# Performance work log

Measured on AMD Instinct MI355X. Metric: run time of the kernel, lower is better.

## Reference

```python
import jax, jax.numpy as jnp
import numpy as np

B, D, L, E, RH, EH = 8192, 1024, 3, 8, 128, 256  # batch, dim, levels, experts, router hidden, expert hidden


def setup_inputs() -> dict:
    key = jax.random.key(0)
    ks = jax.random.split(key, 9)
    s_d = 1.0 / np.sqrt(D)
    s_rh = 1.0 / np.sqrt(RH)
    s_eh = 1.0 / np.sqrt(EH)
    return {
        "x": jax.random.normal(ks[0], (B, D), dtype=jnp.float32),
        # routers: Linear(D,128) -> ReLU -> Linear(128,E) -> softmax, one per level
        "router_w1": jax.random.uniform(ks[1], (L, D, RH), jnp.float32, -s_d, s_d),
        "router_b1": jax.random.uniform(ks[2], (L, RH), jnp.float32, -s_d, s_d),
        "router_w2": jax.random.uniform(ks[3], (L, RH, E), jnp.float32, -s_rh, s_rh),
        "router_b2": jax.random.uniform(ks[4], (L, E), jnp.float32, -s_rh, s_rh),
        # experts: Linear(D,256) -> ReLU -> Linear(256,D), E per level
        "expert_w1": jax.random.uniform(ks[5], (L, E, D, EH), jnp.float32, -s_d, s_d),
        "expert_b1": jax.random.uniform(ks[6], (L, E, EH), jnp.float32, -s_d, s_d),
        "expert_w2": jax.random.uniform(ks[7], (L, E, EH, D), jnp.float32, -s_eh, s_eh),
        "expert_b2": jax.random.uniform(ks[8], (L, E, D), jnp.float32, -s_eh, s_eh),
    }


def _forward(x, router_w1, router_b1, router_w2, router_b2,
             expert_w1, expert_b1, expert_w2, expert_b2):
    def level(cur, params):
        rw1, rb1, rw2, rb2, ew1, eb1, ew2, eb2 = params
        # router: [B,E] softmax weights
        rh = jax.nn.relu(cur @ rw1 + rb1)
        w = jax.nn.softmax(rh @ rw2 + rb2, axis=-1)
        # dense all-expert eval: grouped GEMMs
        h = jax.nn.relu(jnp.einsum("bd,edh->beh", cur, ew1) + eb1)  # [B,E,EH]
        y = jnp.einsum("beh,ehd->bed", h, ew2) + eb2                # [B,E,D]
        out = jnp.einsum("be,bed->bd", w, y)                        # softmax-weighted sum
        return out, None

    out, _ = jax.lax.scan(
        level, x,
        (router_w1, router_b1, router_w2, router_b2,
         expert_w1, expert_b1, expert_w2, expert_b2))
    return out


def reference(x, router_w1, router_b1, router_w2, router_b2,
              expert_w1, expert_b1, expert_w2, expert_b2):
    return _forward(x, router_w1, router_b1, router_w2, router_b2,
                    expert_w1, expert_b1, expert_w2, expert_b2)
```

## Files before the change

kernel.cpp:

```cpp
#include <hip/hip_runtime.h>
#include <stdint.h>

#define BB   8192
#define DD   1024
#define EE   8
#define RHH  128
#define EHH  256
#define NE1  2048
#define KX   2112

using f32x4  = __attribute__((ext_vector_type(4))) float;
using bf16x8 = __attribute__((ext_vector_type(8))) __bf16;

__device__ __forceinline__ unsigned short f2bf(float f) {
    union { float f; uint32_t u; } v; v.f = f;
    uint32_t u = v.u;
    uint32_t r = (u + 0x7FFFu + ((u >> 16) & 1u)) >> 16;
    return (unsigned short)r;
}
__device__ __forceinline__ float bf2f(unsigned short h) {
    union { uint32_t u; float f; } v; v.u = ((uint32_t)h) << 16;
    return v.f;
}

__device__ __forceinline__ void llds16(void* l, const void* g) {
    __builtin_amdgcn_global_load_lds(
        (const __attribute__((address_space(1))) uint32_t*)g,
        (__attribute__((address_space(3))) uint32_t*)l, 16, 0, 0);
}

__device__ __forceinline__ void rawbar() {
    asm volatile("" ::: "memory");
    __builtin_amdgcn_s_barrier();
    asm volatile("" ::: "memory");
}

template<int N> __device__ __forceinline__ void vmwait() {
    asm volatile("s_waitcnt vmcnt(%0)" :: "n"(N) : "memory");
}

#define MFMA16(a,b,c) __builtin_amdgcn_mfma_f32_16x16x32_bf16(a,b,c,0,0,0)

__device__ __forceinline__ void prep512(float (*T)[65], int pbid, int tid,
    const float* __restrict__ rw1, const float* __restrict__ ew1,
    const float* __restrict__ ew2, const float* __restrict__ eb2,
    unsigned short* __restrict__ rw1t, unsigned short* __restrict__ W1t,
    unsigned short* __restrict__ W2t)
{
    const int hl = tid & 63, gq = tid >> 6;
    if (pbid < 512) {
        int e = pbid >> 6, kt = (pbid >> 2) & 15, ht = pbid & 3;
        const float* src = ew1 + ((size_t)e << 18);
#pragma unroll
        for (int i = 0; i < 8; ++i) {
            int kl = i * 8 + gq;
            T[kl][hl] = src[(size_t)(kt * 64 + kl) * 256 + ht * 64 + hl];
        }
        __syncthreads();
#pragma unroll
        for (int i = 0; i < 8; ++i) {
            int hl2 = i * 8 + gq;
            int n = e * 256 + ht * 64 + hl2;
            W1t[(size_t)n * 1024 + kt * 64 + hl] = f2bf(T[hl][hl2]);
        }
    } else if (pbid < 1024) {
        int b2 = pbid - 512;
        int npt = b2 >> 4, dt = b2 & 15;
#pragma unroll
        for (int i = 0; i < 8; ++i) {
            int npl = i * 8 + gq;
            T[npl][hl] = ew2[(size_t)(npt * 64 + npl) * 1024 + dt * 64 + hl];
        }
        __syncthreads();
#pragma unroll
        for (int i = 0; i < 8; ++i) {
            int dl2 = i * 8 + gq;
            int d = dt * 64 + dl2;
            W2t[(size_t)d * KX + npt * 64 + hl] = f2bf(T[hl][dl2]);
        }
    } else if (pbid < 1056) {
        int b2 = pbid - 1024;
        int dt = b2 >> 1, ht = b2 & 1;
#pragma unroll
        for (int i = 0; i < 8; ++i) {
            int dl = i * 8 + gq;
            T[dl][hl] = rw1[(size_t)(dt * 64 + dl) * 128 + ht * 64 + hl];
        }
        __syncthreads();
#pragma unroll
        for (int i = 0; i < 8; ++i) {
            int hl2 = i * 8 + gq;
            int h = ht * 64 + hl2;
            rw1t[(size_t)h * 1024 + dt * 64 + hl] = f2bf(T[hl][hl2]);
        }
    } else if (pbid < 1058) {
        int d = (pbid - 1056) * 512 + tid;
        unsigned short vv[8];
#pragma unroll
        for (int e = 0; e < 8; ++e) vv[e] = f2bf(eb2[(size_t)e * 1024 + d]);
        *(uint4*)&W2t[(size_t)d * KX + NE1] = *(const uint4*)vv;
    } else {
        int d = (pbid - 1058) * 512 + tid;
        uint4 z = make_uint4(0, 0, 0, 0);
#pragma unroll
        for (int j = 0; j < 7; ++j)
            *(uint4*)&W2t[(size_t)d * KX + NE1 + 8 + j * 8] = z;
    }
}

__global__ __launch_bounds__(512) void mega0(
    const float* __restrict__ x, unsigned short* __restrict__ xb,
    unsigned short* __restrict__ Hb,
    const float* __restrict__ rw1, const float* __restrict__ ew1,
    const float* __restrict__ ew2, const float* __restrict__ eb2,
    unsigned short* __restrict__ rw1t, unsigned short* __restrict__ W1t,
    unsigned short* __restrict__ W2t)
{
    __shared__ float T[64][65];
    const int bid = blockIdx.x, tid = threadIdx.x;
    if (bid < 2048) {
        size_t idx = (size_t)bid * 512 + tid;
        const float* p = x + idx * 8;
        uint32_t w[4];
#pragma unroll
        for (int j = 0; j < 4; ++j)
            w[j] = (uint32_t)f2bf(p[2 * j]) | ((uint32_t)f2bf(p[2 * j + 1]) << 16);
        *(uint4*)(xb + idx * 8) = make_uint4(w[0], w[1], w[2], w[3]);
    } else if (bid < 2064) {
        int row = (bid - 2048) * 512 + tid;
        uint4 z = make_uint4(0, 0, 0, 0);
        unsigned short* p = Hb + (size_t)row * KX + NE1 + EE;
#pragma unroll
        for (int j = 0; j < 7; ++j)
            *(uint4*)(p + j * 8) = z;
    } else {
        prep512(T, bid - 2064, tid, rw1, ew1, ew2, eb2, rw1t, W1t, W2t);
    }
}

__global__ __launch_bounds__(512) void prep_lvl512(
    const float* __restrict__ rw1, const float* __restrict__ ew1,
    const float* __restrict__ ew2, const float* __restrict__ eb2,
    unsigned short* __restrict__ rw1t, unsigned short* __restrict__ W1t,
    unsigned short* __restrict__ W2t)
{
    __shared__ float T[64][65];
    prep512(T, blockIdx.x, threadIdx.x, rw1, ew1, ew2, eb2, rw1t, W1t, W2t);
}

__global__ __launch_bounds__(512, 2) void router_prep(
    const unsigned short* __restrict__ xb, const unsigned short* __restrict__ rw1t,
    const float* __restrict__ rw2, const float* __restrict__ rb1,
    const float* __restrict__ rb2, float* __restrict__ wbuf,
    unsigned short* __restrict__ Hb,
    const float* __restrict__ rw1_n, const float* __restrict__ ew1_n,
    const float* __restrict__ ew2_n, const float* __restrict__ eb2_n,
    unsigned short* __restrict__ rw1t_n, unsigned short* __restrict__ W1t_n,
    unsigned short* __restrict__ W2t_n)
{
    __shared__ __align__(16) char SR[73728];
    const int bid = blockIdx.x;
    const int tid = threadIdx.x;

    if (bid >= 128) {
        prep512((float (*)[65])SR, bid - 128, tid, rw1_n, ew1_n, ew2_n, eb2_n,
                rw1t_n, W1t_n, W2t_n);
        return;
    }

    const int lane = tid & 63, wv = tid >> 6;
    const int g = wv >> 2, wq = wv & 3;
    const int l16 = lane & 15, lhi = lane >> 4;
    const long m0 = (long)bid * 64;

    const int r0 = tid >> 2, sl = tid & 3;
    const int sg = sl ^ ((r0 >> 1) & 3);

    const int xrow = (tid >> 2) & 63, xkg = tid >> 8;
    const char* xsrc = (const char*)xb + (m0 + xrow) * 2048 + xkg * 1024 + sg * 16;
    const char* wsrc = (const char*)rw1t + (long)r0 * 2048 + sg * 16;

    f32x4 acc[8];
    const f32x4 zero = {0.f, 0.f, 0.f, 0.f};
#pragma unroll
    for (int i = 0; i < 8; ++i) acc[i] = zero;

    auto stage = [&](int buf, int t) {
        char* base = SR + buf * 24576;
        llds16(base + tid * 16, xsrc + t * 64);
        llds16(base + 8192 + tid * 16, wsrc + t * 64);
        llds16(base + 16384 + tid * 16, wsrc + 1024 + t * 64);
    };

    stage(0, 0); stage(1, 1);

    const int swz = (l16 >> 1) & 3;
    const int aoff = g * 2048 + (wq * 16 + l16) * 32 + ((lhi ^ swz) << 3);
    const int boff = 4096 + g * 4096 + l16 * 32 + ((lhi ^ swz) << 3);

    int cb = 0, sb = 2;
    for (int t = 0; t < 16; ++t) {
        if (t < 15) vmwait<3>(); else vmwait<0>();
        rawbar();
        const unsigned short* bufp = (const unsigned short*)(SR + cb * 24576);
        bf16x8 aF = *(const bf16x8*)&bufp[aoff];
        bf16x8 bF[8];
#pragma unroll
        for (int ni = 0; ni < 8; ++ni)
            bF[ni] = *(const bf16x8*)&bufp[boff + ni * 512];
        if (t + 2 < 16) stage(sb, t + 2);
        __builtin_amdgcn_s_setprio(1);
#pragma unroll
        for (int ni = 0; ni < 8; ++ni)
            acc[ni] = MFMA16(aF, bF[ni], acc[ni]);
        __builtin_amdgcn_s_setprio(0);
        cb = (cb + 1 == 3) ? 0 : cb + 1;
        sb = (sb + 1 == 3) ? 0 : sb + 1;
    }

    rawbar();

    float* rhs = (float*)SR;
    float* lg  = (float*)(SR + 64 * 132 * 4);

    if (g == 1) {
#pragma unroll
        for (int ni = 0; ni < 8; ++ni)
#pragma unroll
            for (int rr = 0; rr < 4; ++rr)
                rhs[(wq * 16 + lhi * 4 + rr) * 132 + ni * 16 + l16] = acc[ni][rr];
    }
    rawbar();
    if (g == 0) {
#pragma unroll
        for (int ni = 0; ni < 8; ++ni) {
            float bv = rb1[ni * 16 + l16];
#pragma unroll
            for (int rr = 0; rr < 4; ++rr) {
                int row = wq * 16 + lhi * 4 + rr, col = ni * 16 + l16;
                float v = acc[ni][rr] + rhs[row * 132 + col] + bv;
                rhs[row * 132 + col] = fmaxf(v, 0.f);
            }
        }
    }
    rawbar();

    {
        const int row = tid & 63, e = tid >> 6;
        float a2 = rb2[e];
        for (int h = 0; h < 128; ++h)
            a2 += rhs[row * 132 + h] * rw2[h * 8 + e];
        lg[row * 9 + e] = a2;
    }
    rawbar();

    if (tid < 64) {
        const int row = tid;
        float l[8], m = -1e30f;
#pragma unroll
        for (int e = 0; e < 8; ++e) { l[e] = lg[row * 9 + e]; m = fmaxf(m, l[e]); }
        float s = 0.f;
#pragma unroll
        for (int e = 0; e < 8; ++e) { l[e] = expf(l[e] - m); s += l[e]; }
        float inv = 1.f / s;
        const long gr = m0 + row;
#pragma unroll
        for (int e = 0; e < 8; ++e) {
            float w = l[e] * inv;
            wbuf[gr * 8 + e] = w;
            Hb[gr * KX + NE1 + e] = f2bf(w);
        }
    }
}

template<int BNv, int BKv, int NBUF, int WNv, int EPI>
__global__ __launch_bounds__(512, 2)
void gemmT(const unsigned short* __restrict__ A, const unsigned short* __restrict__ Bt,
           void* __restrict__ C, const float* __restrict__ bias,
           const float* __restrict__ wrow,
           int K, int lda, int ldb, int ldc)
{
    constexpr int KH  = BKv / 32;
    constexpr int WMv = 8 / WNv;
    constexpr int MR  = 256 / WMv;
    constexpr int NC  = BNv / WNv;
    constexpr int MI  = MR / 16;
    constexpr int NI  = NC / 16;
    constexpr int NCH = 16 / MI;
    constexpr int ALP = 2;
    constexpr int BLP = (BNv * 64) / 8192;
    constexpr int LPT = KH * (ALP + BLP);
    constexpr int SD  = NBUF - 1;
    constexpr int AKH = 256 * 32;
    constexpr int BKH = BNv * 32;

    __shared__ __align__(16) unsigned short As[NBUF * KH * AKH];
    __shared__ __align__(16) unsigned short Bs[NBUF * KH * BKH];

    const int tid = threadIdx.x;
    const int lane = tid & 63, wv = tid >> 6;
    const int wr = wv / WNv, wc = wv % WNv;
    const int l16 = lane & 15, lhi = lane >> 4;
    const long bm0 = (long)blockIdx.x * 256;
    const long bn0 = (long)blockIdx.y * BNv;

    const int r0 = tid >> 2, sl = tid & 3;
    const int sg = sl ^ ((r0 >> 1) & 3);

    const char* aSrc[ALP];
    const char* bSrc[BLP];
#pragma unroll
    for (int a = 0; a < ALP; ++a)
        aSrc[a] = (const char*)A + (bm0 + a * 128 + r0) * (long)lda * 2 + sg * 16;
#pragma unroll
    for (int b = 0; b < BLP; ++b)
        bSrc[b] = (const char*)Bt + (bn0 + b * 128 + r0) * (long)ldb * 2 + sg * 16;

    f32x4 acc[MI][NI];
    const f32x4 zero = {0.f, 0.f, 0.f, 0.f};
#pragma unroll
    for (int i = 0; i < MI; ++i)
#pragma unroll
        for (int j = 0; j < NI; ++j)
            acc[i][j] = zero;

    auto stage = [&](int buf, int t) {
        const int cbyte = t * (BKv * 2);
#pragma unroll
        for (int kh = 0; kh < KH; ++kh) {
            char* ad = (char*)As + ((buf * KH + kh) * AKH) * 2 + tid * 16;
            char* bd = (char*)Bs + ((buf * KH + kh) * BKH) * 2 + tid * 16;
#pragma unroll
            for (int a = 0; a < ALP; ++a)
                llds16(ad + a * 8192, aSrc[a] + cbyte + kh * 64);
#pragma unroll
            for (int b = 0; b < BLP; ++b)
                llds16(bd + b * 8192, bSrc[b] + cbyte + kh * 64);
        }
    };

    const int nt = K / BKv;
#pragma unroll
    for (int p = 0; p < SD; ++p) stage(p, p);

    const int swz = (l16 >> 1) & 3;
    const int aoff = (wr * MR + l16) * 32 + ((lhi ^ swz) << 3);
    const int boff = (wc * NC + l16) * 32 + ((lhi ^ swz) << 3);

    int cb = 0, sb = SD % NBUF;
    for (int t = 0; t < nt; ++t) {
        const int rem = nt - 1 - t;
        if (rem >= SD - 1) vmwait<LPT * (SD - 1)>();
        else if constexpr (SD >= 3) {
            if (rem == 1) vmwait<LPT>(); else vmwait<0>();
        } else vmwait<0>();
        rawbar();

        bf16x8 aF[KH][MI], bF[KH][NI];
#pragma unroll
        for (int kh = 0; kh < KH; ++kh) {
            const unsigned short* ap = &As[(cb * KH + kh) * AKH];
            const unsigned short* bp = &Bs[(cb * KH + kh) * BKH];
#pragma unroll
            for (int mi = 0; mi < MI; ++mi)
                aF[kh][mi] = *(const bf16x8*)&ap[aoff + mi * 512];
#pragma unroll
            for (int ni = 0; ni < NI; ++ni)
                bF[kh][ni] = *(const bf16x8*)&bp[boff + ni * 512];
        }

        if (t + SD < nt) stage(sb, t + SD);

#pragma unroll
        for (int kh = 0; kh < KH; ++kh) {
#pragma unroll
            for (int nc0 = 0; nc0 < NI; nc0 += NCH) {
                __builtin_amdgcn_s_setprio(1);
#pragma unroll
                for (int mi = 0; mi < MI; ++mi)
#pragma unroll
                    for (int nj = 0; nj < NCH; ++nj)
                        acc[mi][nc0 + nj] = MFMA16(aF[kh][mi], bF[kh][nc0 + nj],
                                                   acc[mi][nc0 + nj]);
                __builtin_amdgcn_s_setprio(0);
            }
        }

        cb = (cb + 1 == NBUF) ? 0 : cb + 1;
        sb = (sb + 1 == NBUF) ? 0 : sb + 1;
    }

#pragma unroll
    for (int mi = 0; mi < MI; ++mi) {
#pragma unroll
        for (int ni = 0; ni < NI; ++ni) {
            const long gn = bn0 + wc * NC + ni * 16 + l16;
            float bv = 0.f;
            if (EPI == 1) bv = bias[gn];
#pragma unroll
            for (int rr = 0; rr < 4; ++rr) {
                const long gm = bm0 + wr * MR + mi * 16 + lhi * 4 + rr;
                float v = acc[mi][ni][rr];
                if (EPI == 1) {
                    v = fmaxf(v + bv, 0.f) * wrow[gm * 8 + (int)(gn >> 8)];
                    ((unsigned short*)C)[gm * (long)ldc + gn] = f2bf(v);
                } else if (EPI == 2) {
                    ((unsigned short*)C)[gm * (long)ldc + gn] = f2bf(v);
                } else {
                    ((float*)C)[gm * (long)ldc + gn] = v;
                }
            }
        }
    }
}


extern "C" void kernel_launch(void* const* d_in, const int* in_sizes, int n_in,
                              void* d_out, int out_size, void* d_ws, size_t ws_size,
                              hipStream_t stream) {
    (void)in_sizes; (void)n_in; (void)out_size;
    const float* x   = (const float*)d_in[0];
    const float* rw1 = (const float*)d_in[1];
    const float* rb1 = (const float*)d_in[2];
    const float* rw2 = (const float*)d_in[3];
    const float* rb2 = (const float*)d_in[4];
    const float* ew1 = (const float*)d_in[5];
    const float* eb1 = (const float*)d_in[6];
    const float* ew2 = (const float*)d_in[7];
    const float* eb2 = (const float*)d_in[8];

    const bool dbuf = ws_size >= 69206016u;

    char* ws = (char*)d_ws;
    unsigned short* xb   = (unsigned short*)(ws);
    float*          wbuf = (float*)         (ws + 16777216);
    unsigned short* Hb   = (unsigned short*)(ws + 17039360);
    size_t off = 51642368;
    unsigned short* rw1tb[2];
    unsigned short* W1tb[2];
    unsigned short* W2tb[2];
    rw1tb[0] = (unsigned short*)(ws + off);
    rw1tb[1] = dbuf ? (unsigned short*)(ws + off + 262144) : rw1tb[0];
    off += (dbuf ? 2u : 1u) * 262144u;
    W1tb[0] = (unsigned short*)(ws + off);
    W1tb[1] = dbuf ? (unsigned short*)(ws + off + 4194304) : W1tb[0];
    off += (dbuf ? 2u : 1u) * 4194304u;
    W2tb[0] = (unsigned short*)(ws + off);
    W2tb[1] = dbuf ? (unsigned short*)(ws + off + 4325376) : W2tb[0];

    mega0<<<3124, 512, 0, stream>>>(x, xb, Hb, rw1, ew1, ew2, eb2,
                                    rw1tb[0], W1tb[0], W2tb[0]);

    for (int l = 0; l < 3; ++l) {
        const int b  = dbuf ? (l & 1) : 0;
        const int nb = dbuf ? (b ^ 1) : 0;
        const int ln = (l + 1 < 3) ? (l + 1) : 0;

        if (!dbuf && l > 0)
            prep_lvl512<<<1060, 512, 0, stream>>>(rw1 + (size_t)l * DD * RHH,
                                                  ew1 + (size_t)l * EE * DD * EHH,
                                                  ew2 + (size_t)l * EE * EHH * DD,
                                                  eb2 + (size_t)l * EE * DD,
                                                  rw1tb[0], W1tb[0], W2tb[0]);

        const int rp_grid = (dbuf && l < 2) ? 1188 : 128;
        router_prep<<<rp_grid, 512, 0, stream>>>(
            xb, rw1tb[b],
            rw2 + (size_t)l * RHH * EE, rb1 + (size_t)l * RHH, rb2 + (size_t)l * EE,
            wbuf, Hb,
            rw1 + (size_t)ln * DD * RHH, ew1 + (size_t)ln * EE * DD * EHH,
            ew2 + (size_t)ln * EE * EHH * DD, eb2 + (size_t)ln * EE * DD,
            rw1tb[nb], W1tb[nb], W2tb[nb]);

        gemmT<256, 32, 4, 4, 1><<<dim3(32, 8), 512, 0, stream>>>(
            xb, W1tb[b], Hb, eb1 + (size_t)l * NE1, wbuf, DD, DD, DD, KX);

        if (l < 2)
            gemmT<128, 64, 3, 2, 2><<<dim3(32, 8), 512, 0, stream>>>(
                Hb, W2tb[b], xb, nullptr, nullptr, KX, KX, KX, DD);
        else
            gemmT<128, 64, 3, 2, 3><<<dim3(32, 8), 512, 0, stream>>>(
                Hb, W2tb[b], d_out, nullptr, nullptr, KX, KX, KX, DD);
    }
}
```

Measured before the change: 273.2 us.

## Replace templated 256-row GEMM with smaller 128x128 tile, 256-thread kernel

Swaps the templated 512-thread GEMM (256-row tiles, 256x256 or 256x128 output) for a fixed 256-thread kernel computing 128x128 tiles with BK=32 and a 4-stage LDS ring. Grids grow from 256 blocks to 1024 and 512 blocks, which should fill the 256 CUs better and reduce wave quantization. The cost is lower data reuse per block, so more global and LDS traffic per flop, plus shorter K steps.

```diff
diff --git a/kernel.cpp b/kernel.cpp
--- a/kernel.cpp
+++ b/kernel.cpp
@@ -273,133 +273,102 @@
     }
 }
 
-template<int BNv, int BKv, int NBUF, int WNv, int EPI>
-__global__ __launch_bounds__(512, 2)
-void gemmT(const unsigned short* __restrict__ A, const unsigned short* __restrict__ Bt,
+template<int EPI>
+__global__ __launch_bounds__(256, 2)
+void gemmS(const unsigned short* __restrict__ A, const unsigned short* __restrict__ Bt,
            void* __restrict__ C, const float* __restrict__ bias,
            const float* __restrict__ wrow,
            int K, int lda, int ldb, int ldc)
 {
-    constexpr int KH  = BKv / 32;
-    constexpr int WMv = 8 / WNv;
-    constexpr int MR  = 256 / WMv;
-    constexpr int NC  = BNv / WNv;
-    constexpr int MI  = MR / 16;
-    constexpr int NI  = NC / 16;
-    constexpr int NCH = 16 / MI;
-    constexpr int ALP = 2;
-    constexpr int BLP = (BNv * 64) / 8192;
-    constexpr int LPT = KH * (ALP + BLP);
-    constexpr int SD  = NBUF - 1;
-    constexpr int AKH = 256 * 32;
-    constexpr int BKH = BNv * 32;
-
-    __shared__ __align__(16) unsigned short As[NBUF * KH * AKH];
-    __shared__ __align__(16) unsigned short Bs[NBUF * KH * BKH];
+    constexpr int NBUF = 4, LPT = 4, SD = 3;
+
+    __shared__ __align__(16) unsigned short As[NBUF * 4096];
+    __shared__ __align__(16) unsigned short Bs[NBUF * 4096];
 
     const int tid = threadIdx.x;
     const int lane = tid & 63, wv = tid >> 6;
-    const int wr = wv / WNv, wc = wv % WNv;
+    const int wr = wv >> 1, wc = wv & 1;
     const int l16 = lane & 15, lhi = lane >> 4;
-    const long bm0 = (long)blockIdx.x * 256;
-    const long bn0 = (long)blockIdx.y * BNv;
-
-    const int r0 = tid >> 2, sl = tid & 3;
-    const int sg = sl ^ ((r0 >> 1) & 3);
-
-    const char* aSrc[ALP];
-    const char* bSrc[BLP];
-#pragma unroll
-    for (int a = 0; a < ALP; ++a)
-        aSrc[a] = (const char*)A + (bm0 + a * 128 + r0) * (long)lda * 2 + sg * 16;
-#pragma unroll
-    for (int b = 0; b < BLP; ++b)
-        bSrc[b] = (const char*)Bt + (bn0 + b * 128 + r0) * (long)ldb * 2 + sg * 16;
-
-    f32x4 acc[MI][NI];
+    const long bm0 = (long)blockIdx.x * 128;
+    const long bn0 = (long)blockIdx.y * 128;
+
+    const int sg = (tid & 3) ^ ((tid >> 3) & 3);
+
+    const char* aSrc[2];
+    const char* bSrc[2];
+#pragma unroll
+    for (int a = 0; a < 2; ++a) {
+        aSrc[a] = (const char*)A + (bm0 + a * 64 + (tid >> 2)) * (long)lda * 2 + sg * 16;
+        bSrc[a] = (const char*)Bt + (bn0 + a * 64 + (tid >> 2)) * (long)ldb * 2 + sg * 16;
+    }
+
+    f32x4 acc[4][4];
     const f32x4 zero = {0.f, 0.f, 0.f, 0.f};
 #pragma unroll
-    for (int i = 0; i < MI; ++i)
-#pragma unroll
-        for (int j = 0; j < NI; ++j)
+    for (int i = 0; i < 4; ++i)
+#pragma unroll
+        for (int j = 0; j < 4; ++j)
             acc[i][j] = zero;
 
     auto stage = [&](int buf, int t) {
-        const int cbyte = t * (BKv * 2);
-#pragma unroll
-        for (int kh = 0; kh < KH; ++kh) {
-            char* ad = (char*)As + ((buf * KH + kh) * AKH) * 2 + tid * 16;
-            char* bd = (char*)Bs + ((buf * KH + kh) * BKH) * 2 + tid * 16;
-#pragma unroll
-            for (int a = 0; a < ALP; ++a)
-                llds16(ad + a * 8192, aSrc[a] + cbyte + kh * 64);
-#pragma unroll
-            for (int b = 0; b < BLP; ++b)
-                llds16(bd + b * 8192, bSrc[b] + cbyte + kh * 64);
+        const int cbyte = t * 64;
+#pragma unroll
+        for (int a = 0; a < 2; ++a) {
+            llds16((char*)As + buf * 8192 + a * 4096 + tid * 16, aSrc[a] + cbyte);
+            llds16((char*)Bs + buf * 8192 + a * 4096 + tid * 16, bSrc[a] + cbyte);
         }
     };
 
-    const int nt = K / BKv;
+    const int nt = K / 32;
 #pragma unroll
     for (int p = 0; p < SD; ++p) stage(p, p);
 
-    const int swz = (l16 >> 1) & 3;
-    const int aoff = (wr * MR + l16) * 32 + ((lhi ^ swz) << 3);
-    const int boff = (wc * NC + l16) * 32 + ((lhi ^ swz) << 3);
+    const int swzo = (lhi ^ ((l16 >> 1) & 3)) << 3;
+    const int aoff = (wr * 64 + l16) * 32 + swzo;
+    const int boff = (wc * 64 + l16) * 32 + swzo;
 
     int cb = 0, sb = SD % NBUF;
     for (int t = 0; t < nt; ++t) {
         const int rem = nt - 1 - t;
         if (rem >= SD - 1) vmwait<LPT * (SD - 1)>();
-        else if constexpr (SD >= 3) {
-            if (rem == 1) vmwait<LPT>(); else vmwait<0>();
-        } else vmwait<0>();
+        else if (rem == 1) vmwait<LPT>();
+        else vmwait<0>();
         rawbar();
 
-        bf16x8 aF[KH][MI], bF[KH][NI];
-#pragma unroll
-        for (int kh = 0; kh < KH; ++kh) {
-            const unsigned short* ap = &As[(cb * KH + kh) * AKH];
-            const unsigned short* bp = &Bs[(cb * KH + kh) * BKH];
-#pragma unroll
-            for (int mi = 0; mi < MI; ++mi)
-                aF[kh][mi] = *(const bf16x8*)&ap[aoff + mi * 512];
-#pragma unroll
-            for (int ni = 0; ni < NI; ++ni)
-                bF[kh][ni] = *(const bf16x8*)&bp[boff + ni * 512];
-        }
+        bf16x8 aF[4], bF[4];
+        const unsigned short* ap = &As[cb * 4096];
+        const unsigned short* bp = &Bs[cb * 4096];
+#pragma unroll
+        for (int mi = 0; mi < 4; ++mi)
+            aF[mi] = *(const bf16x8*)&ap[aoff + mi * 512];
+#pragma unroll
+        for (int ni = 0; ni < 4; ++ni)
+            bF[ni] = *(const bf16x8*)&bp[boff + ni * 512];
 
         if (t + SD < nt) stage(sb, t + SD);
 
-#pragma unroll
-        for (int kh = 0; kh < KH; ++kh) {
-#pragma unroll
-            for (int nc0 = 0; nc0 < NI; nc0 += NCH) {
-                __builtin_amdgcn_s_setprio(1);
-#pragma unroll
-                for (int mi = 0; mi < MI; ++mi)
-#pragma unroll
-                    for (int nj = 0; nj < NCH; ++nj)
-                        acc[mi][nc0 + nj] = MFMA16(aF[kh][mi], bF[kh][nc0 + nj],
-                                                   acc[mi][nc0 + nj]);
-                __builtin_amdgcn_s_setprio(0);
-            }
-        }
+        __builtin_amdgcn_s_setprio(1);
+#pragma unroll
+        for (int mi = 0; mi < 4; ++mi)
+#pragma unroll
+            for (int ni = 0; ni < 4; ++ni)
+                acc[mi][ni] = MFMA16(aF[mi], bF[ni], acc[mi][ni]);
+        __builtin_amdgcn_s_setprio(0);
 
         cb = (cb + 1 == NBUF) ? 0 : cb + 1;
         sb = (sb + 1 == NBUF) ? 0 : sb + 1;
     }
 
 #pragma unroll
-    for (int mi = 0; mi < MI; ++mi) {
-#pragma unroll
-        for (int ni = 0; ni < NI; ++ni) {
-            const long gn = bn0 + wc * NC + ni * 16 + l16;
+    for (int mi = 0; mi < 4; ++mi) {
+#pragma unroll
+        for (int ni = 0; ni < 4; ++ni) {
+            const long gn = bn0 + wc * 64 + ni * 16 + l16;
             float bv = 0.f;
             if (EPI == 1) bv = bias[gn];
 #pragma unroll
             for (int rr = 0; rr < 4; ++rr) {
-                const long gm = bm0 + wr * MR + mi * 16 + lhi * 4 + rr;
+                const long gm = bm0 + wr * 64 + mi * 16 + lhi * 4 + rr;
                 float v = acc[mi][ni][rr];
                 if (EPI == 1) {
                     v = fmaxf(v + bv, 0.f) * wrow[gm * 8 + (int)(gn >> 8)];
@@ -472,14 +441,14 @@
             ew2 + (size_t)ln * EE * EHH * DD, eb2 + (size_t)ln * EE * DD,
             rw1tb[nb], W1tb[nb], W2tb[nb]);
 
-        gemmT<256, 32, 4, 4, 1><<<dim3(32, 8), 512, 0, stream>>>(
+        gemmS<1><<<dim3(64, 16), 256, 0, stream>>>(
             xb, W1tb[b], Hb, eb1 + (size_t)l * NE1, wbuf, DD, DD, DD, KX);
 
         if (l < 2)
-            gemmT<128, 64, 3, 2, 2><<<dim3(32, 8), 512, 0, stream>>>(
+            gemmS<2><<<dim3(64, 8), 256, 0, stream>>>(
                 Hb, W2tb[b], xb, nullptr, nullptr, KX, KX, KX, DD);
         else
-            gemmT<128, 64, 3, 2, 3><<<dim3(32, 8), 512, 0, stream>>>(
+            gemmS<3><<<dim3(64, 8), 256, 0, stream>>>(
                 Hb, W2tb[b], d_out, nullptr, nullptr, KX, KX, KX, DD);
     }
 }
```

New measurement: 311.1 us. +13.9%, slower.
